# Optimization experiments

Hardware: AMD Instinct MI355X
Metric: run time of the kernel (lower is better)

Reference implementation:

```python
import jax, jax.numpy as jnp
import numpy as np

R_MIN = 0.1
R_MAX = 2.0

B, N, K = 8, 8192, 100  # batch, atoms, max neighbors


def setup_inputs() -> dict:
    key = jax.random.key(0)
    k1, k2, k3, k4, k5 = jax.random.split(key, 5)
    positions = jax.random.normal(k1, (B, N, 3), dtype=jnp.float32)
    cell = jax.random.normal(k2, (B, 3, 3), dtype=jnp.float32)
    offsets = jax.random.normal(k3, (B, N, K, 3), dtype=jnp.float32)
    neighbors = jax.random.randint(k4, (B, N, K), 0, N, dtype=jnp.int64)
    mask = jax.random.randint(k5, (B, N, K), 0, 2, dtype=jnp.int32)
    return {"positions": positions, "cell": cell, "offsets": offsets,
            "neighbors": neighbors, "mask": mask}


def reference(positions, cell, offsets, neighbors, mask):
    # gather neighbor positions: [B, N, K, 3]
    pos_j = jax.vmap(lambda p, n: p[n])(positions, neighbors)
    # fractional offsets -> cartesian: offsets @ cell per batch
    pos_j = pos_j + jnp.einsum('bnkd,bdc->bnkc', offsets, cell)
    vec = pos_j - positions[:, :, None, :]          # [B, N, K, 3]
    sq = jnp.sum(vec * vec, axis=-1)                # [B, N, K]
    valid = mask > 0
    sq_safe = jnp.where(valid, sq, 1.0)
    d = jnp.where(valid, jnp.sqrt(sq_safe), 0.0)    # masked distances = 0
    # f = 1/d^2, zeroed where d < r_min or d > r_max (masked entries have d=0 < r_min)
    keep = (d >= R_MIN) & (d <= R_MAX)
    f = jnp.where(keep, 1.0 / sq_safe, 0.0)
    return jnp.sum(f, axis=(1, 2)) * 0.5            # [B]
```

## Files before the change

kernel.cpp:

```cpp
#include <hip/hip_runtime.h>
#include <hip/hip_fp16.h>

typedef int          __attribute__((ext_vector_type(2))) i32x2;
typedef float        __attribute__((ext_vector_type(2))) f32x2;
typedef float        __attribute__((ext_vector_type(4))) f32x4;
typedef unsigned int __attribute__((ext_vector_type(2))) u32x2;

constexpr int B_ = 8;
constexpr int N_ = 8192;
constexpr int K_ = 100;
constexpr int PER_BATCH = N_ * K_;
constexpr int THREADS = 1024;
constexpr int NWAVES = THREADS / 64;
constexpr int BLOCKS_PER_BATCH = 32;
constexpr int GRID = B_ * BLOCKS_PER_BATCH;
constexpr int ELEMS_PER_BLOCK = PER_BATCH / BLOCKS_PER_BATCH;
constexpr int TILE_E = 2048;
constexpr int NFULL = 12;
constexpr int TAIL_E = ELEMS_PER_BLOCK - NFULL * TILE_E;
constexpr int NTILES = NFULL + 1;

constexpr float RMIN2 = 0.01f;
constexpr float RMAX2 = 4.0f;

__device__ __forceinline__ u32x2 pack_pos(float x, float y, float z) {
    const unsigned hx = __half_as_ushort(__float2half_rn(x));
    const unsigned hy = __half_as_ushort(__float2half_rn(y));
    const unsigned hz = __half_as_ushort(__float2half_rn(z));
    u32x2 r; r.x = hx | (hy << 16); r.y = hz;
    return r;
}

struct StreamBuf {
    int   nb[TILE_E];
    int   mk[TILE_E];
    float off[3 * TILE_E];
};

__global__ __launch_bounds__(THREADS, 1)
void repulsive_prior_kernel(const float* __restrict__ positions,
                            const float* __restrict__ cell,
                            const float* __restrict__ offsets,
                            const int*   __restrict__ neighbors,
                            const int*   __restrict__ mask,
                            float* __restrict__ out)
{
    __shared__ u32x2 spos[N_];
    __shared__ StreamBuf sbuf[2];
    __shared__ float wsum[NWAVES];

    const int bid   = blockIdx.x;
    const int b     = bid & 7;
    const int chunk = bid >> 3;
    const int t     = (int)threadIdx.x;
    const int wid   = t >> 6;
    const int lane  = t & 63;

    const float* __restrict__ pos_b = positions + (size_t)b * N_ * 3;
    const float* __restrict__ off_b = offsets   + (size_t)b * PER_BATCH * 3;
    const int*   __restrict__ nb_b  = neighbors + (size_t)b * PER_BATCH;
    const int*   __restrict__ mk_b  = mask      + (size_t)b * PER_BATCH;

    const int Ebase0 = chunk * ELEMS_PER_BLOCK;

    auto dma = [&](int bi, int Eb, int ne) {
        StreamBuf* sb = &sbuf[bi];
        const int nbc   = ne >> 8;
        const int total = 5 * nbc;
        for (int c = wid; c < total; c += NWAVES) {
            const int* gsrc;
            int* ldst;
            if (c < nbc) {
                gsrc = nb_b + Eb + (c << 8);
                ldst = &sb->nb[c << 8];
            } else if (c < 2 * nbc) {
                gsrc = mk_b + Eb + ((c - nbc) << 8);
                ldst = &sb->mk[(c - nbc) << 8];
            } else {
                gsrc = (const int*)(off_b + 3 * (size_t)Eb) + ((c - 2 * nbc) << 8);
                ldst = (int*)&sb->off[(c - 2 * nbc) << 8];
            }
            __builtin_amdgcn_global_load_lds(
                (const __attribute__((address_space(1))) unsigned int*)(gsrc + lane * 4),
                (__attribute__((address_space(3))) unsigned int*)ldst,
                16, 0, 0);
        }
    };

    dma(0, Ebase0, TILE_E);

    #pragma unroll
    for (int g0 = 0; g0 < 2; ++g0) {
        const int g = g0 * THREADS + t;
        const f32x4 v0 = *(const f32x4*)(pos_b + 12 * (size_t)g);
        const f32x4 v1 = *(const f32x4*)(pos_b + 12 * (size_t)g + 4);
        const f32x4 v2 = *(const f32x4*)(pos_b + 12 * (size_t)g + 8);
        spos[4 * g + 0] = pack_pos(v0.x, v0.y, v0.z);
        spos[4 * g + 1] = pack_pos(v0.w, v1.x, v1.y);
        spos[4 * g + 2] = pack_pos(v1.z, v1.w, v2.x);
        spos[4 * g + 3] = pack_pos(v2.y, v2.z, v2.w);
    }
    __syncthreads();

    const float* cb = cell + b * 9;
    const float c00 = cb[0], c01 = cb[1], c02 = cb[2];
    const float c10 = cb[3], c11 = cb[4], c12 = cb[5];
    const float c20 = cb[6], c21 = cb[7], c22 = cb[8];

    auto ldpos = [&](int row, float& x, float& y, float& z) {
        const u32x2 v = spos[row];
        x = __half2float(__ushort_as_half((unsigned short)(v.x & 0xffffu)));
        y = __half2float(__ushort_as_half((unsigned short)(v.x >> 16)));
        z = __half2float(__ushort_as_half((unsigned short)(v.y & 0xffffu)));
    };

    float acc = 0.0f;
    auto elem = [&](int Ei, int m, int j, float o0, float o1, float o2) {
        const int n = Ei / 100;
        float pix, piy, piz, pjx, pjy, pjz;
        ldpos(n, pix, piy, piz);
        ldpos(j, pjx, pjy, pjz);
        const float vx = pjx + o0 * c00 + o1 * c10 + o2 * c20 - pix;
        const float vy = pjy + o0 * c01 + o1 * c11 + o2 * c21 - piy;
        const float vz = pjz + o0 * c02 + o1 * c12 + o2 * c22 - piz;
        const float sq = vx * vx + vy * vy + vz * vz;
        const bool keep = (m > 0) & (sq >= RMIN2) & (sq <= RMAX2);
        acc += keep ? (1.0f / sq) : 0.0f;
    };

    #pragma unroll 1
    for (int k = 0; k < NTILES; ++k) {
        if (k < NTILES - 1)
            dma((k + 1) & 1, Ebase0 + (k + 1) * TILE_E,
                (k + 1 == NFULL) ? TAIL_E : TILE_E);

        StreamBuf* sb = &sbuf[k & 1];
        const int ne = (k == NFULL) ? TAIL_E : TILE_E;
        const int e0 = 2 * t;
        if (e0 < ne) {
            const i32x2 nb2 = *(const i32x2*)&sb->nb[e0];
            const i32x2 mk2 = *(const i32x2*)&sb->mk[e0];
            const f32x2 o01 = *(const f32x2*)&sb->off[3 * e0];
            const f32x2 o23 = *(const f32x2*)&sb->off[3 * e0 + 2];
            const f32x2 o45 = *(const f32x2*)&sb->off[3 * e0 + 4];
            const int Ei = Ebase0 + k * TILE_E + e0;
            elem(Ei,     mk2.x, nb2.x, o01.x, o01.y, o23.x);
            elem(Ei + 1, mk2.y, nb2.y, o23.y, o45.x, o45.y);
        }
        __syncthreads();
    }

    #pragma unroll
    for (int off = 32; off > 0; off >>= 1)
        acc += __shfl_down(acc, off, 64);

    if (lane == 0) wsum[wid] = acc;
    __syncthreads();
    if (t == 0) {
        float s = 0.0f;
        #pragma unroll
        for (int w = 0; w < NWAVES; ++w) s += wsum[w];
        atomicAdd(&out[b], 0.5f * s);
    }
}

extern "C" void kernel_launch(void* const* d_in, const int* in_sizes, int n_in,
                              void* d_out, int out_size, void* d_ws, size_t ws_size,
                              hipStream_t stream) {
    const float* positions = (const float*)d_in[0];
    const float* cell      = (const float*)d_in[1];
    const float* offsets   = (const float*)d_in[2];
    const int*   neighbors = (const int*)d_in[3];
    const int*   mask      = (const int*)d_in[4];
    float* out = (float*)d_out;

    (void)hipMemsetAsync(out, 0, out_size * sizeof(float), stream);

    repulsive_prior_kernel<<<GRID, THREADS, 0, stream>>>(
        positions, cell, offsets, neighbors, mask, out);
}
```

Measured before the change: 33.67 us.

## Deepen LDS prefetch to four buffers with explicit vmcnt waits

Replaces the double-buffered 2048-element tile stream with a four-buffer ring of 1024-element tiles, keeping three tiles in flight. A fixed subset of waves issues the global-to-LDS loads, and each iteration waits with a manual s_waitcnt vmcnt plus a raw s_barrier in place of __syncthreads. Each thread now handles one element per tile, and the tail-tile special case goes away. The goal is to hide memory latency with deeper prefetch, at the cost of relying on the hand-written vmcnt count being correct for other threads' DMA completion and on the tile count dividing the block's work evenly.

```diff
diff --git a/kernel.cpp b/kernel.cpp
--- a/kernel.cpp
+++ b/kernel.cpp
@@ -1,8 +1,6 @@
 #include <hip/hip_runtime.h>
 #include <hip/hip_fp16.h>
 
-typedef int          __attribute__((ext_vector_type(2))) i32x2;
-typedef float        __attribute__((ext_vector_type(2))) f32x2;
 typedef float        __attribute__((ext_vector_type(4))) f32x4;
 typedef unsigned int __attribute__((ext_vector_type(2))) u32x2;
 
@@ -15,10 +13,9 @@
 constexpr int BLOCKS_PER_BATCH = 32;
 constexpr int GRID = B_ * BLOCKS_PER_BATCH;
 constexpr int ELEMS_PER_BLOCK = PER_BATCH / BLOCKS_PER_BATCH;
-constexpr int TILE_E = 2048;
-constexpr int NFULL = 12;
-constexpr int TAIL_E = ELEMS_PER_BLOCK - NFULL * TILE_E;
-constexpr int NTILES = NFULL + 1;
+constexpr int TILE_E = 1024;
+constexpr int NTILES = ELEMS_PER_BLOCK / TILE_E;
+constexpr int NBUF = 4;
 
 constexpr float RMIN2 = 0.01f;
 constexpr float RMAX2 = 4.0f;
@@ -46,7 +43,7 @@
                             float* __restrict__ out)
 {
     __shared__ u32x2 spos[N_];
-    __shared__ StreamBuf sbuf[2];
+    __shared__ StreamBuf sbuf[NBUF];
     __shared__ float wsum[NWAVES];
 
     const int bid   = blockIdx.x;
@@ -63,31 +60,32 @@
 
     const int Ebase0 = chunk * ELEMS_PER_BLOCK;
 
-    auto dma = [&](int bi, int Eb, int ne) {
-        StreamBuf* sb = &sbuf[bi];
-        const int nbc   = ne >> 8;
-        const int total = 5 * nbc;
-        for (int c = wid; c < total; c += NWAVES) {
-            const int* gsrc;
-            int* ldst;
-            if (c < nbc) {
-                gsrc = nb_b + Eb + (c << 8);
-                ldst = &sb->nb[c << 8];
-            } else if (c < 2 * nbc) {
-                gsrc = mk_b + Eb + ((c - nbc) << 8);
-                ldst = &sb->mk[(c - nbc) << 8];
-            } else {
-                gsrc = (const int*)(off_b + 3 * (size_t)Eb) + ((c - 2 * nbc) << 8);
-                ldst = (int*)&sb->off[(c - 2 * nbc) << 8];
+    auto dma_tile = [&](int bi, int tileIdx) {
+        if (wid < 10) {
+            StreamBuf* sb = &sbuf[bi];
+            const int Eb = Ebase0 + tileIdx * TILE_E;
+            #pragma unroll
+            for (int s = 0; s < 2; ++s) {
+                const int c = 2 * wid + s;
+                const int* gsrc;
+                int* ldst;
+                if (c < 4)      { gsrc = nb_b + Eb + (c << 8);
+                                  ldst = &sb->nb[c << 8]; }
+                else if (c < 8) { gsrc = mk_b + Eb + ((c - 4) << 8);
+                                  ldst = &sb->mk[(c - 4) << 8]; }
+                else            { gsrc = (const int*)(off_b + 3 * (size_t)Eb) + ((c - 8) << 8);
+                                  ldst = (int*)&sb->off[(c - 8) << 8]; }
+                __builtin_amdgcn_global_load_lds(
+                    (const __attribute__((address_space(1))) unsigned int*)(gsrc + lane * 4),
+                    (__attribute__((address_space(3))) unsigned int*)ldst,
+                    16, 0, 0);
             }
-            __builtin_amdgcn_global_load_lds(
-                (const __attribute__((address_space(1))) unsigned int*)(gsrc + lane * 4),
-                (__attribute__((address_space(3))) unsigned int*)ldst,
-                16, 0, 0);
         }
     };
 
-    dma(0, Ebase0, TILE_E);
+    dma_tile(0, 0);
+    dma_tile(1, 1);
+    dma_tile(2, 2);
 
     #pragma unroll
     for (int g0 = 0; g0 < 2; ++g0) {
@@ -115,8 +113,27 @@
     };
 
     float acc = 0.0f;
-    auto elem = [&](int Ei, int m, int j, float o0, float o1, float o2) {
-        const int n = Ei / 100;
+
+    #pragma unroll 1
+    for (int k = 0; k < NTILES; ++k) {
+        if (k > 0) {
+            asm volatile("s_waitcnt vmcnt(4)" ::: "memory");
+            __builtin_amdgcn_sched_barrier(0);
+            __builtin_amdgcn_s_barrier();
+        }
+        if (k + 3 < NTILES)
+            dma_tile((k + 3) & 3, k + 3);
+        __builtin_amdgcn_sched_barrier(0);
+
+        const StreamBuf* sb = &sbuf[k & 3];
+        const int j  = sb->nb[t];
+        const int m  = sb->mk[t];
+        const float o0 = sb->off[3 * t + 0];
+        const float o1 = sb->off[3 * t + 1];
+        const float o2 = sb->off[3 * t + 2];
+        const int Ei = Ebase0 + k * TILE_E + t;
+        const int n  = Ei / 100;
+
         float pix, piy, piz, pjx, pjy, pjz;
         ldpos(n, pix, piy, piz);
         ldpos(j, pjx, pjy, pjz);
@@ -126,28 +143,6 @@
         const float sq = vx * vx + vy * vy + vz * vz;
         const bool keep = (m > 0) & (sq >= RMIN2) & (sq <= RMAX2);
         acc += keep ? (1.0f / sq) : 0.0f;
-    };
-
-    #pragma unroll 1
-    for (int k = 0; k < NTILES; ++k) {
-        if (k < NTILES - 1)
-            dma((k + 1) & 1, Ebase0 + (k + 1) * TILE_E,
-                (k + 1 == NFULL) ? TAIL_E : TILE_E);
-
-        StreamBuf* sb = &sbuf[k & 1];
-        const int ne = (k == NFULL) ? TAIL_E : TILE_E;
-        const int e0 = 2 * t;
-        if (e0 < ne) {
-            const i32x2 nb2 = *(const i32x2*)&sb->nb[e0];
-            const i32x2 mk2 = *(const i32x2*)&sb->mk[e0];
-            const f32x2 o01 = *(const f32x2*)&sb->off[3 * e0];
-            const f32x2 o23 = *(const f32x2*)&sb->off[3 * e0 + 2];
-            const f32x2 o45 = *(const f32x2*)&sb->off[3 * e0 + 4];
-            const int Ei = Ebase0 + k * TILE_E + e0;
-            elem(Ei,     mk2.x, nb2.x, o01.x, o01.y, o23.x);
-            elem(Ei + 1, mk2.y, nb2.y, o23.y, o45.x, o45.y);
-        }
-        __syncthreads();
     }
 
     #pragma unroll
```

Result: faster. 31.34 us (-6.9%).
